# Kernel tuning notes

Hardware: AMD Instinct MI355X
Metric: run time of the kernel (lower is better)

The kernel has to match this reference:

```python
import jax, jax.numpy as jnp
import numpy as np

N_NODES = 8192


def _gcn_norm(edge_index, num_nodes):
    # PyG GCNConv default: add self-loops, symmetric normalization.
    src, dst = edge_index[0], edge_index[1]
    loop = jnp.arange(num_nodes, dtype=src.dtype)
    src = jnp.concatenate([src, loop])
    dst = jnp.concatenate([dst, loop])
    deg = jax.ops.segment_sum(jnp.ones_like(dst, dtype=jnp.float32), dst,
                              num_segments=num_nodes)
    dis = jnp.where(deg > 0, jax.lax.rsqrt(jnp.maximum(deg, 1.0)), 0.0)
    norm = dis[src] * dis[dst]  # [E + N]
    return src, dst, norm


def _gcn_conv(x, W, b, src, dst, norm, num_nodes):
    h = x @ W                           # [N, F_out] dense GEMM
    msg = h[src] * norm[:, None]        # gather + scale, [E+N, F_out]
    out = jax.ops.segment_sum(msg, dst, num_segments=num_nodes)  # scatter-add
    return out + b


def setup_inputs() -> dict:
    key = jax.random.key(0)
    ks = jax.random.split(key, 8)
    N, E, F_in, H1, H2, F_out = N_NODES, 65536, 512, 4096, 1024, 10
    x = jax.random.normal(ks[0], (N, F_in), dtype=jnp.float32)
    edge_index = jax.random.randint(ks[1], (2, E), 0, N, dtype=jnp.int64)
    # Glorot-ish scaled weights
    W1 = jax.random.normal(ks[2], (F_in, H1), dtype=jnp.float32) * (1.0 / np.sqrt(F_in))
    b1 = jnp.zeros((H1,), dtype=jnp.float32)
    W2 = jax.random.normal(ks[3], (H1, H2), dtype=jnp.float32) * (1.0 / np.sqrt(H1))
    b2 = jnp.zeros((H2,), dtype=jnp.float32)
    W3 = jax.random.normal(ks[4], (H2, F_out), dtype=jnp.float32) * (1.0 / np.sqrt(H2))
    b3 = jnp.zeros((F_out,), dtype=jnp.float32)
    return {"x": x, "W1": W1, "b1": b1, "W2": W2, "b2": b2,
            "W3": W3, "b3": b3, "edge_index": edge_index}


def reference(x, W1, b1, W2, b2, W3, b3, edge_index):
    N = N_NODES
    src, dst, norm = _gcn_norm(edge_index, N)
    h = _gcn_conv(x.astype(jnp.float32), W1, b1, src, dst, norm, N)
    h = jax.nn.relu(h)  # dropout is identity in eval mode
    h = _gcn_conv(h, W2, b2, src, dst, norm, N)
    h = jax.nn.relu(h)
    h = _gcn_conv(h, W3, b3, src, dst, norm, N)
    return jax.nn.log_softmax(h, axis=1)
```

## Files before the change

kernel.cpp:

```cpp
#include <hip/hip_runtime.h>
#include <math.h>

#define N_NODES 8192
#define N_EDGES 65536
#define F_IN    512
#define HID1    4096
#define HID2    1024
#define F_OUT   10
#define H3_STRIDE 16
#define W3B_STRIDE 1032

typedef __bf16 bf16x8 __attribute__((ext_vector_type(8)));
typedef float floatx4 __attribute__((ext_vector_type(4)));
typedef float floatx16 __attribute__((ext_vector_type(16)));

static __device__ __forceinline__ unsigned short f2bf(float f) {
    union { float f; unsigned u; } v; v.f = f;
    unsigned r = v.u + 0x7fffu + ((v.u >> 16) & 1u);
    return (unsigned short)(r >> 16);
}
static __device__ __forceinline__ float bf2f(unsigned short u) {
    union { unsigned u; float f; } v; v.u = ((unsigned)u) << 16;
    return v.f;
}
static __device__ __forceinline__ void unpack8(uint4 r, float* f) {
    union { unsigned u; float v; } c;
    c.u = r.x << 16;          f[0] = c.v;
    c.u = r.x & 0xffff0000u;  f[1] = c.v;
    c.u = r.y << 16;          f[2] = c.v;
    c.u = r.y & 0xffff0000u;  f[3] = c.v;
    c.u = r.z << 16;          f[4] = c.v;
    c.u = r.z & 0xffff0000u;  f[5] = c.v;
    c.u = r.w << 16;          f[6] = c.v;
    c.u = r.w & 0xffff0000u;  f[7] = c.v;
}
static __device__ __forceinline__ uint4 pack8(const float* f) {
    uint4 o;
    o.x = (unsigned)f2bf(f[0]) | ((unsigned)f2bf(f[1]) << 16);
    o.y = (unsigned)f2bf(f[2]) | ((unsigned)f2bf(f[3]) << 16);
    o.z = (unsigned)f2bf(f[4]) | ((unsigned)f2bf(f[5]) << 16);
    o.w = (unsigned)f2bf(f[6]) | ((unsigned)f2bf(f[7]) << 16);
    return o;
}

__global__ __launch_bounds__(1024) void hist_scan_kernel(
        const int* __restrict__ ei, int* __restrict__ deg,
        int* __restrict__ row_ptr, int* __restrict__ cnt) {
    __shared__ int hist[N_NODES];
    __shared__ int sums[1024];
    int t = threadIdx.x;
#pragma unroll
    for (int i = 0; i < 8; i++) hist[t + i * 1024] = 0;
    __syncthreads();
#pragma unroll
    for (int i = 0; i < 64; i++) {
        int d = ei[N_EDGES + i * 1024 + t];
        atomicAdd(&hist[d], 1);
    }
    __syncthreads();
    int base = t * 8;
    int local[8], run = 0;
#pragma unroll
    for (int i = 0; i < 8; i++) {
        int dv = hist[base + i];
        deg[base + i] = dv;
        cnt[base + i] = 0;
        local[i] = run; run += dv;
    }
    sums[t] = run;
    __syncthreads();
    for (int off = 1; off < 1024; off <<= 1) {
        int val = (t >= off) ? sums[t - off] : 0;
        __syncthreads();
        sums[t] += val;
        __syncthreads();
    }
    int offset = (t == 0) ? 0 : sums[t - 1];
#pragma unroll
    for (int i = 0; i < 8; i++) row_ptr[base + i] = offset + local[i];
    if (t == 1023) row_ptr[N_NODES] = sums[1023];
}

static __device__ __forceinline__ void transpose_body(
        const float* __restrict__ W, unsigned short* __restrict__ Wt,
        int K, int N, int k0, int n0, int tid, float (*t)[33]) {
    int c = tid & 31, r8 = tid >> 5;
#pragma unroll
    for (int i = 0; i < 4; i++) {
        int r = r8 + i * 8;
        t[r][c] = W[(size_t)(k0 + r) * N + n0 + c];
    }
    __syncthreads();
#pragma unroll
    for (int i = 0; i < 4; i++) {
        int r = r8 + i * 8;
        Wt[(size_t)(n0 + r) * K + k0 + c] = f2bf(t[c][r]);
    }
}

__global__ __launch_bounds__(256) void megaprep_kernel(
        const int* __restrict__ ei, const int* __restrict__ deg,
        const int* __restrict__ row_ptr, int* __restrict__ cnt,
        int* __restrict__ csr_src, float* __restrict__ csr_w,
        const float* __restrict__ x, unsigned short* __restrict__ xb,
        const float* __restrict__ W1, unsigned short* __restrict__ W1t,
        const float* __restrict__ W2, unsigned short* __restrict__ W2t,
        const float* __restrict__ W3, unsigned short* __restrict__ w3b) {
    __shared__ float t[32][33];
    int b = blockIdx.x, tid = threadIdx.x;
    if (b < 256) {
        int e = b * 256 + tid;
        int s = ei[e];
        int d = ei[N_EDGES + e];
        int slot = row_ptr[d] + atomicAdd(&cnt[d], 1);
        csr_src[slot] = s;
        csr_w[slot] = rsqrtf((float)((deg[s] + 1) * (deg[d] + 1)));
    } else if (b < 4352) {
        int i = (b - 256) * 256 + tid;
        float4 a = ((const float4*)x)[i];
        ushort4 o;
        o.x = f2bf(a.x); o.y = f2bf(a.y); o.z = f2bf(a.z); o.w = f2bf(a.w);
        ((ushort4*)xb)[i] = o;
    } else if (b < 6400) {
        int bb = b - 4352;
        transpose_body(W1, W1t, F_IN, HID1, (bb >> 7) * 32, (bb & 127) * 32, tid, t);
    } else if (b < 10496) {
        int bb = b - 6400;
        transpose_body(W2, W2t, HID1, HID2, (bb >> 5) * 32, (bb & 31) * 32, tid, t);
    } else {
        for (int i = tid; i < HID2 * F_OUT; i += 256) {
            int k = i / F_OUT, c = i % F_OUT;
            w3b[c * W3B_STRIDE + k] = f2bf(W3[i]);
        }
    }
}

__global__ __launch_bounds__(256) void agg1_kernel(
        const unsigned short* __restrict__ xb, const int* __restrict__ row_ptr,
        const int* __restrict__ csr_src, const float* __restrict__ csr_w,
        const int* __restrict__ deg, unsigned short* __restrict__ out) {
    int v = blockIdx.x * 4 + (threadIdx.x >> 6);
    int t = threadIdx.x & 63;
    const uint4* xp = (const uint4*)xb;
    float sw = 1.0f / (float)(deg[v] + 1);
    float acc[8], tmp[8];
    unpack8(xp[(size_t)v * 64 + t], tmp);
#pragma unroll
    for (int j = 0; j < 8; j++) acc[j] = sw * tmp[j];
    int e = row_ptr[v], end = row_ptr[v + 1];
    for (; e + 4 <= end; e += 4) {
        int s0 = csr_src[e], s1 = csr_src[e + 1];
        int s2 = csr_src[e + 2], s3 = csr_src[e + 3];
        float w0 = csr_w[e], w1 = csr_w[e + 1];
        float w2 = csr_w[e + 2], w3 = csr_w[e + 3];
        float f0[8], f1[8], f2[8], f3[8];
        unpack8(xp[(size_t)s0 * 64 + t], f0);
        unpack8(xp[(size_t)s1 * 64 + t], f1);
        unpack8(xp[(size_t)s2 * 64 + t], f2);
        unpack8(xp[(size_t)s3 * 64 + t], f3);
#pragma unroll
        for (int j = 0; j < 8; j++)
            acc[j] += w0 * f0[j] + w1 * f1[j] + w2 * f2[j] + w3 * f3[j];
    }
    for (; e < end; e++) {
        int s = csr_src[e];
        float w = csr_w[e];
        float f0[8];
        unpack8(xp[(size_t)s * 64 + t], f0);
#pragma unroll
        for (int j = 0; j < 8; j++) acc[j] += w * f0[j];
    }
    ((uint4*)out)[(size_t)v * 64 + t] = pack8(acc);
}

__global__ __launch_bounds__(256) void agg2_gemm3_kernel(
        const unsigned short* __restrict__ h, const int* __restrict__ row_ptr,
        const int* __restrict__ csr_src, const float* __restrict__ csr_w,
        const int* __restrict__ deg, const float* __restrict__ b2,
        const unsigned short* __restrict__ w3b, float* __restrict__ H3) {
    __shared__ unsigned short w3s[F_OUT * W3B_STRIDE];
    __shared__ float red[4][F_OUT];
    int tid = threadIdx.x;
    for (int i = tid; i < F_OUT * W3B_STRIDE; i += 256) w3s[i] = w3b[i];
    __syncthreads();
    int half = tid >> 7;
    int t = tid & 127;
    int v = blockIdx.x * 2 + half;
    const uint4* hp = (const uint4*)h;
    float sw = 1.0f / (float)(deg[v] + 1);
    float acc[8], tmp[8];
    unpack8(hp[(size_t)v * 128 + t], tmp);
#pragma unroll
    for (int j = 0; j < 8; j++) acc[j] = sw * tmp[j];
    int e = row_ptr[v], end = row_ptr[v + 1];
    for (; e + 4 <= end; e += 4) {
        int s0 = csr_src[e], s1 = csr_src[e + 1];
        int s2 = csr_src[e + 2], s3 = csr_src[e + 3];
        float w0 = csr_w[e], w1 = csr_w[e + 1];
        float w2 = csr_w[e + 2], w3 = csr_w[e + 3];
        float f0[8], f1[8], f2[8], f3[8];
        unpack8(hp[(size_t)s0 * 128 + t], f0);
        unpack8(hp[(size_t)s1 * 128 + t], f1);
        unpack8(hp[(size_t)s2 * 128 + t], f2);
        unpack8(hp[(size_t)s3 * 128 + t], f3);
#pragma unroll
        for (int j = 0; j < 8; j++)
            acc[j] += w0 * f0[j] + w1 * f1[j] + w2 * f2[j] + w3 * f3[j];
    }
    for (; e < end; e++) {
        int s = csr_src[e];
        float w = csr_w[e];
        float f0[8];
        unpack8(hp[(size_t)s * 128 + t], f0);
#pragma unroll
        for (int j = 0; j < 8; j++) acc[j] += w * f0[j];
    }
    float4 b4a = ((const float4*)b2)[t * 2];
    float4 b4b = ((const float4*)b2)[t * 2 + 1];
    acc[0] = fmaxf(acc[0] + b4a.x, 0.0f); acc[1] = fmaxf(acc[1] + b4a.y, 0.0f);
    acc[2] = fmaxf(acc[2] + b4a.z, 0.0f); acc[3] = fmaxf(acc[3] + b4a.w, 0.0f);
    acc[4] = fmaxf(acc[4] + b4b.x, 0.0f); acc[5] = fmaxf(acc[5] + b4b.y, 0.0f);
    acc[6] = fmaxf(acc[6] + b4b.z, 0.0f); acc[7] = fmaxf(acc[7] + b4b.w, 0.0f);

    float partial[F_OUT];
#pragma unroll
    for (int c = 0; c < F_OUT; c++) {
        float wf[8];
        unpack8(*(const uint4*)&w3s[c * W3B_STRIDE + t * 8], wf);
        partial[c] = acc[0] * wf[0] + acc[1] * wf[1] + acc[2] * wf[2] + acc[3] * wf[3]
                   + acc[4] * wf[4] + acc[5] * wf[5] + acc[6] * wf[6] + acc[7] * wf[7];
    }
#pragma unroll
    for (int c = 0; c < F_OUT; c++) {
#pragma unroll
        for (int off = 32; off > 0; off >>= 1)
            partial[c] += __shfl_xor(partial[c], off, 64);
    }
    int wave = tid >> 6, lane = tid & 63;
    if (lane == 0) {
#pragma unroll
        for (int c = 0; c < F_OUT; c++) red[wave][c] = partial[c];
    }
    __syncthreads();
    if (tid < 2 * F_OUT) {
        int hh = tid / F_OUT, c = tid % F_OUT;
        H3[(size_t)(blockIdx.x * 2 + hh) * H3_STRIDE + c] =
            red[hh * 2][c] + red[hh * 2 + 1][c];
    }
}

template <bool OUT_BF16, bool BIAS, bool RELU>
__global__ __launch_bounds__(256) void gemm2_mfma_kernel(
        const unsigned short* __restrict__ A,
        const unsigned short* __restrict__ Bt,
        const float* __restrict__ bias,
        void* __restrict__ C,
        int M, int N, int K) {
    __shared__ unsigned short As[128 * 128];
    __shared__ unsigned short Bs[128 * 128];
    int tid = threadIdx.x;
    int wave = tid >> 6, lane = tid & 63;
    int wm = wave >> 1, wn = wave & 1;
    int GN = N >> 7;
    int b = blockIdx.x;
    int ntile = (b >> 3) % GN;
    int mtile = ((b >> 3) / GN) * 8 + (b & 7);
    int m0 = mtile * 128, n0 = ntile * 128;
    int lrow = lane & 31, lhalf = lane >> 5;

    floatx16 acc[2][2] = {};

    for (int k0 = 0; k0 < K; k0 += 128) {
#pragma unroll
        for (int j = 0; j < 8; j++) {
            int idx = j * 256 + tid;
            int r = idx >> 4;
            int kc = (idx & 15) ^ (r & 15);
            __builtin_amdgcn_global_load_lds(
                (const __attribute__((address_space(1))) void*)(A + (size_t)(m0 + r) * K + k0 + kc * 8),
                (__attribute__((address_space(3))) void*)(&As[idx * 8]), 16, 0, 0);
            __builtin_amdgcn_global_load_lds(
                (const __attribute__((address_space(1))) void*)(Bt + (size_t)(n0 + r) * K + k0 + kc * 8),
                (__attribute__((address_space(3))) void*)(&Bs[idx * 8]), 16, 0, 0);
        }
        __syncthreads();
#pragma unroll
        for (int kk = 0; kk < 8; kk++) {
            bf16x8 af[2], bfr[2];
            int c = kk * 2 + lhalf;
#pragma unroll
            for (int mt = 0; mt < 2; mt++) {
                int R = wm * 64 + mt * 32 + lrow;
                af[mt] = *(const bf16x8*)&As[(R * 16 + (c ^ (R & 15))) * 8];
            }
#pragma unroll
            for (int nt = 0; nt < 2; nt++) {
                int R = wn * 64 + nt * 32 + lrow;
                bfr[nt] = *(const bf16x8*)&Bs[(R * 16 + (c ^ (R & 15))) * 8];
            }
#pragma unroll
            for (int mt = 0; mt < 2; mt++)
#pragma unroll
                for (int nt = 0; nt < 2; nt++)
                    acc[mt][nt] = __builtin_amdgcn_mfma_f32_32x32x16_bf16(
                        af[mt], bfr[nt], acc[mt][nt], 0, 0, 0);
        }
        __syncthreads();
    }

#pragma unroll
    for (int mt = 0; mt < 2; mt++) {
#pragma unroll
        for (int nt = 0; nt < 2; nt++) {
            int col = n0 + wn * 64 + nt * 32 + lrow;
            float bv = BIAS ? bias[col] : 0.0f;
#pragma unroll
            for (int reg = 0; reg < 16; reg++) {
                int row = m0 + wm * 64 + mt * 32 + (reg & 3) + 8 * (reg >> 2) + 4 * lhalf;
                float v = acc[mt][nt][reg] + bv;
                if (RELU) v = fmaxf(v, 0.0f);
                if (OUT_BF16)
                    ((unsigned short*)C)[(size_t)row * N + col] = f2bf(v);
                else
                    ((float*)C)[(size_t)row * N + col] = v;
            }
        }
    }
}

__global__ __launch_bounds__(256, 2) void gemm1_mfma_kernel(
        const unsigned short* __restrict__ A,
        const unsigned short* __restrict__ Bt,
        const float* __restrict__ bias,
        unsigned short* __restrict__ C) {
    __shared__ unsigned short As[256 * 64];
    __shared__ unsigned short Bs[128 * 64];
    const int K = F_IN, N = HID1;
    int tid = threadIdx.x;
    int wave = tid >> 6, lane = tid & 63;
    int wm = wave >> 1, wn = wave & 1;
    int b = blockIdx.x;
    int GN = N >> 7;
    int ntile = (b >> 3) % GN;
    int mtile = ((b >> 3) / GN) * 8 + (b & 7);
    int m0 = mtile * 256, n0 = ntile * 128;
    int lrow = lane & 31, lhalf = lane >> 5;

    floatx16 acc[4][2] = {};

    for (int k0 = 0; k0 < K; k0 += 64) {
#pragma unroll
        for (int j = 0; j < 8; j++) {
            int idx = j * 256 + tid;
            int r = idx >> 3;
            int kc = (idx & 7) ^ (r & 7);
            __builtin_amdgcn_global_load_lds(
                (const __attribute__((address_space(1))) void*)(A + (size_t)(m0 + r) * K + k0 + kc * 8),
                (__attribute__((address_space(3))) void*)(&As[idx * 8]), 16, 0, 0);
        }
#pragma unroll
        for (int j = 0; j < 4; j++) {
            int idx = j * 256 + tid;
            int r = idx >> 3;
            int kc = (idx & 7) ^ (r & 7);
            __builtin_amdgcn_global_load_lds(
                (const __attribute__((address_space(1))) void*)(Bt + (size_t)(n0 + r) * K + k0 + kc * 8),
                (__attribute__((address_space(3))) void*)(&Bs[idx * 8]), 16, 0, 0);
        }
        __syncthreads();
#pragma unroll
        for (int kk = 0; kk < 4; kk++) {
            bf16x8 af[4], bfr[2];
            int c = kk * 2 + lhalf;
#pragma unroll
            for (int mt = 0; mt < 4; mt++) {
                int R = wm * 128 + mt * 32 + lrow;
                af[mt] = *(const bf16x8*)&As[(R * 8 + (c ^ (R & 7))) * 8];
            }
#pragma unroll
            for (int nt = 0; nt < 2; nt++) {
                int R = wn * 64 + nt * 32 + lrow;
                bfr[nt] = *(const bf16x8*)&Bs[(R * 8 + (c ^ (R & 7))) * 8];
            }
#pragma unroll
            for (int mt = 0; mt < 4; mt++)
#pragma unroll
                for (int nt = 0; nt < 2; nt++)
                    acc[mt][nt] = __builtin_amdgcn_mfma_f32_32x32x16_bf16(
                        af[mt], bfr[nt], acc[mt][nt], 0, 0, 0);
        }
        __syncthreads();
    }

#pragma unroll
    for (int mt = 0; mt < 4; mt++) {
#pragma unroll
        for (int nt = 0; nt < 2; nt++) {
            int col = n0 + wn * 64 + nt * 32 + lrow;
            float bv = bias[col];
#pragma unroll
            for (int reg = 0; reg < 16; reg++) {
                int row = m0 + wm * 128 + mt * 32 + (reg & 3) + 8 * (reg >> 2) + 4 * lhalf;
                float v = fmaxf(acc[mt][nt][reg] + bv, 0.0f);
                C[(size_t)row * N + col] = f2bf(v);
            }
        }
    }
}

__global__ void final_kernel(const float* __restrict__ h3, const int* __restrict__ row_ptr,
                             const int* __restrict__ csr_src, const float* __restrict__ csr_w,
                             const int* __restrict__ deg, const float* __restrict__ b3,
                             float* __restrict__ out) {
    int v = blockIdx.x * blockDim.x + threadIdx.x;
    if (v >= N_NODES) return;
    const float4* h4 = (const float4*)h3;
    float sw = 1.0f / (float)(deg[v] + 1);
    float a[12];
    *(float4*)&a[0] = h4[v * 4];
    *(float4*)&a[4] = h4[v * 4 + 1];
    *(float4*)&a[8] = h4[v * 4 + 2];
    float acc[F_OUT];
#pragma unroll
    for (int c = 0; c < F_OUT; c++) acc[c] = b3[c] + sw * a[c];
    int end = row_ptr[v + 1];
    for (int e = row_ptr[v]; e < end; e++) {
        int s = csr_src[e];
        float w = csr_w[e];
        float bsrc[12];
        *(float4*)&bsrc[0] = h4[s * 4];
        *(float4*)&bsrc[4] = h4[s * 4 + 1];
        *(float4*)&bsrc[8] = h4[s * 4 + 2];
#pragma unroll
        for (int c = 0; c < F_OUT; c++) acc[c] += w * bsrc[c];
    }
    float m = acc[0];
#pragma unroll
    for (int c = 1; c < F_OUT; c++) m = fmaxf(m, acc[c]);
    float ssum = 0.0f;
#pragma unroll
    for (int c = 0; c < F_OUT; c++) ssum += expf(acc[c] - m);
    float l = logf(ssum);
#pragma unroll
    for (int c = 0; c < F_OUT; c++) out[v * F_OUT + c] = acc[c] - m - l;
}

extern "C" void kernel_launch(void* const* d_in, const int* in_sizes, int n_in,
                              void* d_out, int out_size, void* d_ws, size_t ws_size,
                              hipStream_t stream) {
    const float* x  = (const float*)d_in[0];
    const float* W1 = (const float*)d_in[1];
    const float* b1 = (const float*)d_in[2];
    const float* W2 = (const float*)d_in[3];
    const float* b2 = (const float*)d_in[4];
    const float* W3 = (const float*)d_in[5];
    const float* b3 = (const float*)d_in[6];
    const int*   ei = (const int*)d_in[7];
    float* out = (float*)d_out;

    char* p = (char*)d_ws;
    int*   deg     = (int*)p;    p += N_NODES * 4;
    int*   cnt     = (int*)p;    p += N_NODES * 4;
    int*   row_ptr = (int*)p;    p += 33024;
    int*   csr_src = (int*)p;    p += N_EDGES * 4;
    float* csr_w   = (float*)p;  p += N_EDGES * 4;
    float* h3      = (float*)p;  p += N_NODES * H3_STRIDE * 4;
    unsigned short* w3b = (unsigned short*)p; p += (F_OUT * W3B_STRIDE * 2 + 255) / 256 * 256;
    unsigned short* xb    = (unsigned short*)p; p += (size_t)N_NODES * F_IN * 2;
    unsigned short* agg_x = (unsigned short*)p; p += (size_t)N_NODES * F_IN * 2;
    unsigned short* W1t   = (unsigned short*)p; p += (size_t)HID1 * F_IN * 2;
    unsigned short* W2t   = (unsigned short*)p; p += (size_t)HID2 * HID1 * 2;
    unsigned short* h1    = (unsigned short*)p; p += (size_t)N_NODES * HID1 * 2;
    unsigned short* h2pre = (unsigned short*)p; p += (size_t)N_NODES * HID2 * 2;

    hist_scan_kernel<<<1, 1024, 0, stream>>>(ei, deg, row_ptr, cnt);
    megaprep_kernel<<<10497, 256, 0, stream>>>(ei, deg, row_ptr, cnt, csr_src, csr_w,
                                               x, xb, W1, W1t, W2, W2t, W3, w3b);

    agg1_kernel<<<N_NODES / 4, 256, 0, stream>>>(xb, row_ptr, csr_src, csr_w, deg, agg_x);
    gemm1_mfma_kernel<<<(HID1 / 128) * (N_NODES / 256), 256, 0, stream>>>(agg_x, W1t, b1, h1);

    gemm2_mfma_kernel<true, false, false><<<(HID2 / 128) * (N_NODES / 128), 256, 0, stream>>>(
        h1, W2t, nullptr, h2pre, N_NODES, HID2, HID1);

    agg2_gemm3_kernel<<<N_NODES / 2, 256, 0, stream>>>(h2pre, row_ptr, csr_src, csr_w,
                                                       deg, b2, w3b, h3);

    final_kernel<<<N_NODES / 256, 256, 0, stream>>>(h3, row_ptr, csr_src, csr_w, deg, b3, out);
}
```

Measured before the change: 287.2 us.

## Replace both GEMMs with a triple-buffered pipelined 128x256 MFMA kernel

Merges the two GEMM kernels into one 512-thread kernel with 128x256 tiles and BK=64. It uses a three-stage LDS ring buffer where global-to-LDS loads for tile t+2 are issued while tile t is computed, tracked with explicit vmcnt waits and raw barriers. It also adds an XCD-aware block swizzle and raises wave priority around the MFMA calls. The aim is to hide global load latency and remove the two full syncs per k-step, at the cost of 144KB of LDS per block (one block per CU) and fragile hand-written waitcnt logic.

After: 297.7 us. +3.7%, slower.

```diff
diff --git a/kernel.cpp b/kernel.cpp
--- a/kernel.cpp
+++ b/kernel.cpp
@@ -249,160 +249,116 @@
     }
 }
 
+#define GP_STAGE(t_, q_) do {                                                  \
+    unsigned short* As_ = lds + (q_) * 24576;                                  \
+    unsigned short* Bs_ = As_ + 8192;                                          \
+    int k0_ = (t_) * 64;                                                       \
+    _Pragma("unroll")                                                          \
+    for (int j = 0; j < 2; j++) {              \
+        int idx = j * 512 + tid;                                               \
+        int r = idx >> 3;                                                      \
+        int kc = (idx & 7) ^ (r & 7);                                          \
+        __builtin_amdgcn_global_load_lds(                                      \
+            (const __attribute__((address_space(1))) void*)(Abase + (size_t)r * K + k0_ + kc * 8), \
+            (__attribute__((address_space(3))) void*)(&As_[idx * 8]), 16, 0, 0); \
+    }                                                                          \
+    _Pragma("unroll")                                                          \
+    for (int j = 0; j < 4; j++) {              \
+        int idx = j * 512 + tid;                                               \
+        int r = idx >> 3;                                                      \
+        int kc = (idx & 7) ^ (r & 7);                                          \
+        __builtin_amdgcn_global_load_lds(                                      \
+            (const __attribute__((address_space(1))) void*)(Bbase + (size_t)r * K + k0_ + kc * 8), \
+            (__attribute__((address_space(3))) void*)(&Bs_[idx * 8]), 16, 0, 0); \
+    }                                                                          \
+} while (0)
+
 template <bool OUT_BF16, bool BIAS, bool RELU>
-__global__ __launch_bounds__(256) void gemm2_mfma_kernel(
+__global__ __launch_bounds__(512) void gemm_pipe_kernel(
         const unsigned short* __restrict__ A,
         const unsigned short* __restrict__ Bt,
         const float* __restrict__ bias,
         void* __restrict__ C,
         int M, int N, int K) {
-    __shared__ unsigned short As[128 * 128];
-    __shared__ unsigned short Bs[128 * 128];
+    __shared__ unsigned short lds[3 * 24576];
     int tid = threadIdx.x;
     int wave = tid >> 6, lane = tid & 63;
-    int wm = wave >> 1, wn = wave & 1;
-    int GN = N >> 7;
+    int wm = wave & 1, wn = wave >> 1;
+    int lrow = lane & 31, lhalf = lane >> 5;
+
+    int nwg = gridDim.x;
+    int cpx = nwg >> 3;
     int b = blockIdx.x;
-    int ntile = (b >> 3) % GN;
-    int mtile = ((b >> 3) / GN) * 8 + (b & 7);
-    int m0 = mtile * 128, n0 = ntile * 128;
-    int lrow = lane & 31, lhalf = lane >> 5;
+    int swz = (b & 7) * cpx + (b >> 3);
+    int nm = M >> 7;
+    int ntile = swz / nm;
+    int mtile = swz - ntile * nm;
+
+    const unsigned short* Abase = A + (size_t)mtile * 128 * K;
+    const unsigned short* Bbase = Bt + (size_t)ntile * 256 * K;
 
     floatx16 acc[2][2] = {};
-
-    for (int k0 = 0; k0 < K; k0 += 128) {
-#pragma unroll
-        for (int j = 0; j < 8; j++) {
-            int idx = j * 256 + tid;
-            int r = idx >> 4;
-            int kc = (idx & 15) ^ (r & 15);
-            __builtin_amdgcn_global_load_lds(
-                (const __attribute__((address_space(1))) void*)(A + (size_t)(m0 + r) * K + k0 + kc * 8),
-                (__attribute__((address_space(3))) void*)(&As[idx * 8]), 16, 0, 0);
-            __builtin_amdgcn_global_load_lds(
-                (const __attribute__((address_space(1))) void*)(Bt + (size_t)(n0 + r) * K + k0 + kc * 8),
-                (__attribute__((address_space(3))) void*)(&Bs[idx * 8]), 16, 0, 0);
-        }
-        __syncthreads();
-#pragma unroll
-        for (int kk = 0; kk < 8; kk++) {
+    int NT = K >> 6;
+
+    GP_STAGE(0, 0);
+    GP_STAGE(1, 1);
+    asm volatile("s_waitcnt vmcnt(6)" ::: "memory");
+    __builtin_amdgcn_s_barrier();
+
+    int q = 0, qn = 2;
+    for (int t = 0; t < NT; t++) {
+        unsigned short* As_ = lds + q * 24576;
+        unsigned short* Bs_ = As_ + 8192;
+#pragma unroll
+        for (int kk = 0; kk < 4; kk++) {
             bf16x8 af[2], bfr[2];
             int c = kk * 2 + lhalf;
 #pragma unroll
             for (int mt = 0; mt < 2; mt++) {
                 int R = wm * 64 + mt * 32 + lrow;
-                af[mt] = *(const bf16x8*)&As[(R * 16 + (c ^ (R & 15))) * 8];
+                af[mt] = *(const bf16x8*)&As_[(R * 8 + (c ^ (R & 7))) * 8];
             }
 #pragma unroll
             for (int nt = 0; nt < 2; nt++) {
                 int R = wn * 64 + nt * 32 + lrow;
-                bfr[nt] = *(const bf16x8*)&Bs[(R * 16 + (c ^ (R & 15))) * 8];
+                bfr[nt] = *(const bf16x8*)&Bs_[(R * 8 + (c ^ (R & 7))) * 8];
             }
+            if (kk == 0 && t + 2 < NT) {
+                GP_STAGE(t + 2, qn);
+            }
+            __builtin_amdgcn_s_setprio(1);
 #pragma unroll
             for (int mt = 0; mt < 2; mt++)
 #pragma unroll
                 for (int nt = 0; nt < 2; nt++)
                     acc[mt][nt] = __builtin_amdgcn_mfma_f32_32x32x16_bf16(
                         af[mt], bfr[nt], acc[mt][nt], 0, 0, 0);
+            __builtin_amdgcn_s_setprio(0);
         }
-        __syncthreads();
+        if (t + 2 < NT)
+            asm volatile("s_waitcnt vmcnt(6)" ::: "memory");
+        else
+            asm volatile("s_waitcnt vmcnt(0)" ::: "memory");
+        __builtin_amdgcn_s_barrier();
+        q = (q == 2) ? 0 : q + 1;
+        qn = (qn == 2) ? 0 : qn + 1;
     }
 
 #pragma unroll
     for (int mt = 0; mt < 2; mt++) {
 #pragma unroll
         for (int nt = 0; nt < 2; nt++) {
-            int col = n0 + wn * 64 + nt * 32 + lrow;
+            int col = ntile * 256 + wn * 64 + nt * 32 + lrow;
             float bv = BIAS ? bias[col] : 0.0f;
 #pragma unroll
             for (int reg = 0; reg < 16; reg++) {
-                int row = m0 + wm * 64 + mt * 32 + (reg & 3) + 8 * (reg >> 2) + 4 * lhalf;
+                int row = mtile * 128 + wm * 64 + mt * 32 + (reg & 3) + 8 * (reg >> 2) + 4 * lhalf;
                 float v = acc[mt][nt][reg] + bv;
                 if (RELU) v = fmaxf(v, 0.0f);
                 if (OUT_BF16)
                     ((unsigned short*)C)[(size_t)row * N + col] = f2bf(v);
                 else
                     ((float*)C)[(size_t)row * N + col] = v;
-            }
-        }
-    }
-}
-
-__global__ __launch_bounds__(256, 2) void gemm1_mfma_kernel(
-        const unsigned short* __restrict__ A,
-        const unsigned short* __restrict__ Bt,
-        const float* __restrict__ bias,
-        unsigned short* __restrict__ C) {
-    __shared__ unsigned short As[256 * 64];
-    __shared__ unsigned short Bs[128 * 64];
-    const int K = F_IN, N = HID1;
-    int tid = threadIdx.x;
-    int wave = tid >> 6, lane = tid & 63;
-    int wm = wave >> 1, wn = wave & 1;
-    int b = blockIdx.x;
-    int GN = N >> 7;
-    int ntile = (b >> 3) % GN;
-    int mtile = ((b >> 3) / GN) * 8 + (b & 7);
-    int m0 = mtile * 256, n0 = ntile * 128;
-    int lrow = lane & 31, lhalf = lane >> 5;
-
-    floatx16 acc[4][2] = {};
-
-    for (int k0 = 0; k0 < K; k0 += 64) {
-#pragma unroll
-        for (int j = 0; j < 8; j++) {
-            int idx = j * 256 + tid;
-            int r = idx >> 3;
-            int kc = (idx & 7) ^ (r & 7);
-            __builtin_amdgcn_global_load_lds(
-                (const __attribute__((address_space(1))) void*)(A + (size_t)(m0 + r) * K + k0 + kc * 8),
-                (__attribute__((address_space(3))) void*)(&As[idx * 8]), 16, 0, 0);
-        }
-#pragma unroll
-        for (int j = 0; j < 4; j++) {
-            int idx = j * 256 + tid;
-            int r = idx >> 3;
-            int kc = (idx & 7) ^ (r & 7);
-            __builtin_amdgcn_global_load_lds(
-                (const __attribute__((address_space(1))) void*)(Bt + (size_t)(n0 + r) * K + k0 + kc * 8),
-                (__attribute__((address_space(3))) void*)(&Bs[idx * 8]), 16, 0, 0);
-        }
-        __syncthreads();
-#pragma unroll
-        for (int kk = 0; kk < 4; kk++) {
-            bf16x8 af[4], bfr[2];
-            int c = kk * 2 + lhalf;
-#pragma unroll
-            for (int mt = 0; mt < 4; mt++) {
-                int R = wm * 128 + mt * 32 + lrow;
-                af[mt] = *(const bf16x8*)&As[(R * 8 + (c ^ (R & 7))) * 8];
-            }
-#pragma unroll
-            for (int nt = 0; nt < 2; nt++) {
-                int R = wn * 64 + nt * 32 + lrow;
-                bfr[nt] = *(const bf16x8*)&Bs[(R * 8 + (c ^ (R & 7))) * 8];
-            }
-#pragma unroll
-            for (int mt = 0; mt < 4; mt++)
-#pragma unroll
-                for (int nt = 0; nt < 2; nt++)
-                    acc[mt][nt] = __builtin_amdgcn_mfma_f32_32x32x16_bf16(
-                        af[mt], bfr[nt], acc[mt][nt], 0, 0, 0);
-        }
-        __syncthreads();
-    }
-
-#pragma unroll
-    for (int mt = 0; mt < 4; mt++) {
-#pragma unroll
-        for (int nt = 0; nt < 2; nt++) {
-            int col = n0 + wn * 64 + nt * 32 + lrow;
-            float bv = bias[col];
-#pragma unroll
-            for (int reg = 0; reg < 16; reg++) {
-                int row = m0 + wm * 128 + mt * 32 + (reg & 3) + 8 * (reg >> 2) + 4 * lhalf;
-                float v = fmaxf(acc[mt][nt][reg] + bv, 0.0f);
-                C[(size_t)row * N + col] = f2bf(v);
             }
         }
     }
@@ -478,9 +434,10 @@
                                                x, xb, W1, W1t, W2, W2t, W3, w3b);
 
     agg1_kernel<<<N_NODES / 4, 256, 0, stream>>>(xb, row_ptr, csr_src, csr_w, deg, agg_x);
-    gemm1_mfma_kernel<<<(HID1 / 128) * (N_NODES / 256), 256, 0, stream>>>(agg_x, W1t, b1, h1);
-
-    gemm2_mfma_kernel<true, false, false><<<(HID2 / 128) * (N_NODES / 128), 256, 0, stream>>>(
+    gemm_pipe_kernel<true, true, true><<<(N_NODES / 128) * (HID1 / 256), 512, 0, stream>>>(
+        agg_x, W1t, b1, h1, N_NODES, HID1, F_IN);
+
+    gemm_pipe_kernel<true, false, false><<<(N_NODES / 128) * (HID2 / 256), 512, 0, stream>>>(
         h1, W2t, nullptr, h2pre, N_NODES, HID2, HID1);
 
     agg2_gemm3_kernel<<<N_NODES / 2, 256, 0, stream>>>(h2pre, row_ptr, csr_src, csr_w,
```

## Pipeline gemm2 with triple-buffered LDS and larger 256x128 tiles

Applied to the files above, without the earlier changes.

Replaces the single-buffered gemm2 kernel with a triple-buffered version that issues global-to-LDS loads two K-steps ahead and interleaves them with the MFMA work. Each wave now computes 128x64 instead of 64x64, so each B fragment is reused across more A rows, and s_setprio raises priority around the MFMA blocks. Per-block synchronisation now relies on explicit vmcnt waits instead of two __syncthreads per step. The 144KB LDS footprint limits occupancy to one block per CU, and the doubled accumulators raise register pressure.

Measured after the change: 284.1 us. About the same (-1.1%).

```diff
diff --git a/kernel.cpp b/kernel.cpp
--- a/kernel.cpp
+++ b/kernel.cpp
@@ -249,74 +249,114 @@
     }
 }
 
+#define G2_STAGE_A(t_, q_, j0_) do {                                           \
+    unsigned short* As_ = lds + (q_) * 24576;                                  \
+    int k0_ = (t_) * 64;                                                       \
+    _Pragma("unroll")                                                          \
+    for (int j = (j0_); j < (j0_) + 4; j++) {      \
+        int idx = j * 256 + tid;                                               \
+        int r = idx >> 3;                                                      \
+        int kc = (idx & 7) ^ (r & 7);                                          \
+        __builtin_amdgcn_global_load_lds(                                      \
+            (const __attribute__((address_space(1))) void*)(Abase + (size_t)r * K + k0_ + kc * 8), \
+            (__attribute__((address_space(3))) void*)(&As_[idx * 8]), 16, 0, 0); \
+    }                                                                          \
+} while (0)
+
+#define G2_STAGE_B(t_, q_) do {                                                \
+    unsigned short* Bs_ = lds + (q_) * 24576 + 16384;                          \
+    int k0_ = (t_) * 64;                                                       \
+    _Pragma("unroll")                                                          \
+    for (int j = 0; j < 4; j++) {                  \
+        int idx = j * 256 + tid;                                               \
+        int r = idx >> 3;                                                      \
+        int kc = (idx & 7) ^ (r & 7);                                          \
+        __builtin_amdgcn_global_load_lds(                                      \
+            (const __attribute__((address_space(1))) void*)(Bbase + (size_t)r * K + k0_ + kc * 8), \
+            (__attribute__((address_space(3))) void*)(&Bs_[idx * 8]), 16, 0, 0); \
+    }                                                                          \
+} while (0)
+
 template <bool OUT_BF16, bool BIAS, bool RELU>
-__global__ __launch_bounds__(256) void gemm2_mfma_kernel(
+__global__ __launch_bounds__(256, 1) void gemm2_pipe_kernel(
         const unsigned short* __restrict__ A,
         const unsigned short* __restrict__ Bt,
         const float* __restrict__ bias,
         void* __restrict__ C,
         int M, int N, int K) {
-    __shared__ unsigned short As[128 * 128];
-    __shared__ unsigned short Bs[128 * 128];
+    __shared__ unsigned short lds[3 * 24576];
     int tid = threadIdx.x;
     int wave = tid >> 6, lane = tid & 63;
     int wm = wave >> 1, wn = wave & 1;
+    int lrow = lane & 31, lhalf = lane >> 5;
+
     int GN = N >> 7;
     int b = blockIdx.x;
     int ntile = (b >> 3) % GN;
     int mtile = ((b >> 3) / GN) * 8 + (b & 7);
-    int m0 = mtile * 128, n0 = ntile * 128;
-    int lrow = lane & 31, lhalf = lane >> 5;
-
-    floatx16 acc[2][2] = {};
-
-    for (int k0 = 0; k0 < K; k0 += 128) {
-#pragma unroll
-        for (int j = 0; j < 8; j++) {
-            int idx = j * 256 + tid;
-            int r = idx >> 4;
-            int kc = (idx & 15) ^ (r & 15);
-            __builtin_amdgcn_global_load_lds(
-                (const __attribute__((address_space(1))) void*)(A + (size_t)(m0 + r) * K + k0 + kc * 8),
-                (__attribute__((address_space(3))) void*)(&As[idx * 8]), 16, 0, 0);
-            __builtin_amdgcn_global_load_lds(
-                (const __attribute__((address_space(1))) void*)(Bt + (size_t)(n0 + r) * K + k0 + kc * 8),
-                (__attribute__((address_space(3))) void*)(&Bs[idx * 8]), 16, 0, 0);
-        }
-        __syncthreads();
-#pragma unroll
-        for (int kk = 0; kk < 8; kk++) {
-            bf16x8 af[2], bfr[2];
+    int m0 = mtile * 256, n0 = ntile * 128;
+
+    const unsigned short* Abase = A + (size_t)m0 * K;
+    const unsigned short* Bbase = Bt + (size_t)n0 * K;
+
+    floatx16 acc[4][2] = {};
+    int NT = K >> 6;
+
+    G2_STAGE_A(0, 0, 0); G2_STAGE_A(0, 0, 4); G2_STAGE_B(0, 0);
+    G2_STAGE_A(1, 1, 0); G2_STAGE_A(1, 1, 4); G2_STAGE_B(1, 1);
+    asm volatile("s_waitcnt vmcnt(12)" ::: "memory");
+    __builtin_amdgcn_s_barrier();
+
+    int q = 0, qn = 2;
+    for (int t = 0; t < NT; t++) {
+        unsigned short* As_ = lds + q * 24576;
+        unsigned short* Bs_ = As_ + 16384;
+#pragma unroll
+        for (int kk = 0; kk < 4; kk++) {
+            bf16x8 af[4], bfr[2];
             int c = kk * 2 + lhalf;
 #pragma unroll
-            for (int mt = 0; mt < 2; mt++) {
-                int R = wm * 64 + mt * 32 + lrow;
-                af[mt] = *(const bf16x8*)&As[(R * 16 + (c ^ (R & 15))) * 8];
+            for (int mt = 0; mt < 4; mt++) {
+                int R = wm * 128 + mt * 32 + lrow;
+                af[mt] = *(const bf16x8*)&As_[(R * 8 + (c ^ (R & 7))) * 8];
             }
 #pragma unroll
             for (int nt = 0; nt < 2; nt++) {
                 int R = wn * 64 + nt * 32 + lrow;
-                bfr[nt] = *(const bf16x8*)&Bs[(R * 16 + (c ^ (R & 15))) * 8];
-            }
-#pragma unroll
-            for (int mt = 0; mt < 2; mt++)
+                bfr[nt] = *(const bf16x8*)&Bs_[(R * 8 + (c ^ (R & 7))) * 8];
+            }
+            if (t + 2 < NT) {
+                if (kk == 0)      G2_STAGE_A(t + 2, qn, 0);
+                else if (kk == 1) G2_STAGE_A(t + 2, qn, 4);
+                else if (kk == 2) G2_STAGE_B(t + 2, qn);
+            }
+            __builtin_amdgcn_s_setprio(1);
+#pragma unroll
+            for (int mt = 0; mt < 4; mt++)
 #pragma unroll
                 for (int nt = 0; nt < 2; nt++)
                     acc[mt][nt] = __builtin_amdgcn_mfma_f32_32x32x16_bf16(
                         af[mt], bfr[nt], acc[mt][nt], 0, 0, 0);
-        }
-        __syncthreads();
-    }
-
-#pragma unroll
-    for (int mt = 0; mt < 2; mt++) {
+            __builtin_amdgcn_s_setprio(0);
+        }
+        if (t + 2 < NT)
+            asm volatile("s_waitcnt vmcnt(12)" ::: "memory");
+        else
+            asm volatile("s_waitcnt vmcnt(0)" ::: "memory");
+        __builtin_amdgcn_s_barrier();
+        q = (q == 2) ? 0 : q + 1;
+        qn = (qn == 2) ? 0 : qn + 1;
+    }
+
+#pragma unroll
+    for (int mt = 0; mt < 4; mt++) {
 #pragma unroll
         for (int nt = 0; nt < 2; nt++) {
             int col = n0 + wn * 64 + nt * 32 + lrow;
             float bv = BIAS ? bias[col] : 0.0f;
 #pragma unroll
             for (int reg = 0; reg < 16; reg++) {
-                int row = m0 + wm * 64 + mt * 32 + (reg & 3) + 8 * (reg >> 2) + 4 * lhalf;
+                int row = m0 + wm * 128 + mt * 32 + (reg & 3) + 8 * (reg >> 2) + 4 * lhalf;
                 float v = acc[mt][nt][reg] + bv;
                 if (RELU) v = fmaxf(v, 0.0f);
                 if (OUT_BF16)
@@ -480,7 +520,7 @@
     agg1_kernel<<<N_NODES / 4, 256, 0, stream>>>(xb, row_ptr, csr_src, csr_w, deg, agg_x);
     gemm1_mfma_kernel<<<(HID1 / 128) * (N_NODES / 256), 256, 0, stream>>>(agg_x, W1t, b1, h1);
 
-    gemm2_mfma_kernel<true, false, false><<<(HID2 / 128) * (N_NODES / 128), 256, 0, stream>>>(
+    gemm2_pipe_kernel<true, false, false><<<(N_NODES / 256) * (HID2 / 128), 256, 0, stream>>>(
         h1, W2t, nullptr, h2pre, N_NODES, HID2, HID1);
 
     agg2_gemm3_kernel<<<N_NODES / 2, 256, 0, stream>>>(h2pre, row_ptr, csr_src, csr_w,
```

## Replace gemm1 with double-buffered 256x256 pipelined MFMA kernel; vectorize histogram loads

Applied to the files above, without the earlier changes.

Replaces the first GEMM with a 512-thread kernel using 256x256 tiles, double-buffered LDS and global-to-LDS prefetch of the next K slice interleaved with MFMA work. It uses explicit vmcnt waits, s_barrier and setprio, so loads overlap compute instead of a full sync per K step. The degree histogram now reads destination indices as int4 to cut load instructions. The new kernel uses 128KB of LDS per block and fragile manual wait counts, which may limit occupancy or risk races.

New measurement: 284.0 us. Within noise of the previous version (-1.1%).

```diff
diff --git a/kernel.cpp b/kernel.cpp
--- a/kernel.cpp
+++ b/kernel.cpp
@@ -52,10 +52,14 @@
 #pragma unroll
     for (int i = 0; i < 8; i++) hist[t + i * 1024] = 0;
     __syncthreads();
-#pragma unroll
-    for (int i = 0; i < 64; i++) {
-        int d = ei[N_EDGES + i * 1024 + t];
-        atomicAdd(&hist[d], 1);
+    const int4* ei4 = (const int4*)(ei + N_EDGES);
+#pragma unroll
+    for (int i = 0; i < 16; i++) {
+        int4 d4 = ei4[i * 1024 + t];
+        atomicAdd(&hist[d4.x], 1);
+        atomicAdd(&hist[d4.y], 1);
+        atomicAdd(&hist[d4.z], 1);
+        atomicAdd(&hist[d4.w], 1);
     }
     __syncthreads();
     int base = t * 8;
@@ -249,6 +253,118 @@
     }
 }
 
+#define P8_STAGE(mat_, kh_, dd_, base_, k0_) do {                              \
+    unsigned short* L_ = lds + ((dd_) * 4 + (mat_) * 2 + (kh_)) * 8192;        \
+    _Pragma("unroll")                                                          \
+    for (int j = 0; j < 2; j++) {                                              \
+        int slot = j * 512 + tid;                                              \
+        int s4 = slot >> 4, cs = slot & 15;                                    \
+        int csp = cs ^ (s4 & 3);                                               \
+        int grow = s4 * 4 + (csp >> 2);                                        \
+        int gcol = (csp & 3) * 8;                                              \
+        __builtin_amdgcn_global_load_lds(                                      \
+            (const __attribute__((address_space(1))) void*)((base_) + (size_t)grow * K + (k0_) + (kh_) * 32 + gcol), \
+            (__attribute__((address_space(3))) void*)(&L_[slot * 8]), 16, 0, 0); \
+    }                                                                          \
+} while (0)
+
+#define P8_OFF(R_, lc_) ((((R_) >> 2) * 128) + (((((R_) & 3) << 2) | (lc_)) ^ (((R_) >> 2) & 3)) * 8)
+
+__global__ __launch_bounds__(512, 2) void gemm1_pipe8_kernel(
+        const unsigned short* __restrict__ A,
+        const unsigned short* __restrict__ Bt,
+        const float* __restrict__ bias,
+        unsigned short* __restrict__ C) {
+    __shared__ unsigned short lds[65536];
+    const int K = F_IN, N = HID1;
+    int tid = threadIdx.x;
+    int wave = tid >> 6, lane = tid & 63;
+    int wm = wave >> 2, wn = wave & 3;
+    int lrow = lane & 31, lhalf = lane >> 5;
+
+    int b = blockIdx.x;
+    int GN = HID1 >> 8;
+    int ntile = (b >> 3) % GN;
+    int mtile = ((b >> 3) / GN) * 8 + (b & 7);
+    int m0 = mtile * 256, n0 = ntile * 256;
+
+    const unsigned short* Abase = A + (size_t)m0 * K;
+    const unsigned short* Bbase = Bt + (size_t)n0 * K;
+
+    floatx16 acc[4][2] = {};
+    const int NT = K >> 6;
+
+    P8_STAGE(0, 0, 0, Abase, 0);
+    P8_STAGE(1, 0, 0, Bbase, 0);
+    P8_STAGE(0, 1, 0, Abase, 0);
+    P8_STAGE(1, 1, 0, Bbase, 0);
+    asm volatile("s_waitcnt vmcnt(4)" ::: "memory");
+    __builtin_amdgcn_s_barrier();
+
+    for (int t = 0; t < NT; t++) {
+        int d = t & 1, dn = d ^ 1;
+        int k1 = (t + 1) * 64;
+#pragma unroll
+        for (int kk = 0; kk < 4; kk++) {
+            if (kk == 2) {
+                if (t + 1 < NT)
+                    asm volatile("s_waitcnt vmcnt(4)" ::: "memory");
+                else
+                    asm volatile("s_waitcnt vmcnt(0)" ::: "memory");
+                __builtin_amdgcn_s_barrier();
+            }
+            int kh = kk >> 1;
+            int lc0 = (kk & 1) * 2 + lhalf;
+            const unsigned short* Ak = lds + (d * 4 + kh) * 8192;
+            const unsigned short* Bk = lds + (d * 4 + 2 + kh) * 8192;
+            bf16x8 af[4], bfr[2];
+#pragma unroll
+            for (int mt = 0; mt < 4; mt++) {
+                int R = wm * 128 + mt * 32 + lrow;
+                af[mt] = *(const bf16x8*)&Ak[P8_OFF(R, lc0)];
+            }
+#pragma unroll
+            for (int nt = 0; nt < 2; nt++) {
+                int R = wn * 64 + nt * 32 + lrow;
+                bfr[nt] = *(const bf16x8*)&Bk[P8_OFF(R, lc0)];
+            }
+            if (t + 1 < NT) {
+                if (kk == 0)      P8_STAGE(0, 0, dn, Abase, k1);
+                else if (kk == 1) P8_STAGE(1, 0, dn, Bbase, k1);
+                else if (kk == 2) P8_STAGE(0, 1, dn, Abase, k1);
+                else              P8_STAGE(1, 1, dn, Bbase, k1);
+            }
+            __builtin_amdgcn_s_barrier();
+            __builtin_amdgcn_s_setprio(1);
+#pragma unroll
+            for (int mt = 0; mt < 4; mt++)
+#pragma unroll
+                for (int nt = 0; nt < 2; nt++)
+                    acc[mt][nt] = __builtin_amdgcn_mfma_f32_32x32x16_bf16(
+                        af[mt], bfr[nt], acc[mt][nt], 0, 0, 0);
+            __builtin_amdgcn_s_setprio(0);
+            if (kk == 0 || kk == 2) __builtin_amdgcn_s_barrier();
+        }
+        asm volatile("s_waitcnt vmcnt(4)" ::: "memory");
+        __builtin_amdgcn_s_barrier();
+    }
+
+#pragma unroll
+    for (int mt = 0; mt < 4; mt++) {
+#pragma unroll
+        for (int nt = 0; nt < 2; nt++) {
+            int col = n0 + wn * 64 + nt * 32 + lrow;
+            float bv = bias[col];
+#pragma unroll
+            for (int reg = 0; reg < 16; reg++) {
+                int row = m0 + wm * 128 + mt * 32 + (reg & 3) + 8 * (reg >> 2) + 4 * lhalf;
+                float v = fmaxf(acc[mt][nt][reg] + bv, 0.0f);
+                C[(size_t)row * N + col] = f2bf(v);
+            }
+        }
+    }
+}
+
 template <bool OUT_BF16, bool BIAS, bool RELU>
 __global__ __launch_bounds__(256) void gemm2_mfma_kernel(
         const unsigned short* __restrict__ A,
@@ -328,86 +444,6 @@
     }
 }
 
-__global__ __launch_bounds__(256, 2) void gemm1_mfma_kernel(
-        const unsigned short* __restrict__ A,
-        const unsigned short* __restrict__ Bt,
-        const float* __restrict__ bias,
-        unsigned short* __restrict__ C) {
-    __shared__ unsigned short As[256 * 64];
-    __shared__ unsigned short Bs[128 * 64];
-    const int K = F_IN, N = HID1;
-    int tid = threadIdx.x;
-    int wave = tid >> 6, lane = tid & 63;
-    int wm = wave >> 1, wn = wave & 1;
-    int b = blockIdx.x;
-    int GN = N >> 7;
-    int ntile = (b >> 3) % GN;
-    int mtile = ((b >> 3) / GN) * 8 + (b & 7);
-    int m0 = mtile * 256, n0 = ntile * 128;
-    int lrow = lane & 31, lhalf = lane >> 5;
-
-    floatx16 acc[4][2] = {};
-
-    for (int k0 = 0; k0 < K; k0 += 64) {
-#pragma unroll
-        for (int j = 0; j < 8; j++) {
-            int idx = j * 256 + tid;
-            int r = idx >> 3;
-            int kc = (idx & 7) ^ (r & 7);
-            __builtin_amdgcn_global_load_lds(
-                (const __attribute__((address_space(1))) void*)(A + (size_t)(m0 + r) * K + k0 + kc * 8),
-                (__attribute__((address_space(3))) void*)(&As[idx * 8]), 16, 0, 0);
-        }
-#pragma unroll
-        for (int j = 0; j < 4; j++) {
-            int idx = j * 256 + tid;
-            int r = idx >> 3;
-            int kc = (idx & 7) ^ (r & 7);
-            __builtin_amdgcn_global_load_lds(
-                (const __attribute__((address_space(1))) void*)(Bt + (size_t)(n0 + r) * K + k0 + kc * 8),
-                (__attribute__((address_space(3))) void*)(&Bs[idx * 8]), 16, 0, 0);
-        }
-        __syncthreads();
-#pragma unroll
-        for (int kk = 0; kk < 4; kk++) {
-            bf16x8 af[4], bfr[2];
-            int c = kk * 2 + lhalf;
-#pragma unroll
-            for (int mt = 0; mt < 4; mt++) {
-                int R = wm * 128 + mt * 32 + lrow;
-                af[mt] = *(const bf16x8*)&As[(R * 8 + (c ^ (R & 7))) * 8];
-            }
-#pragma unroll
-            for (int nt = 0; nt < 2; nt++) {
-                int R = wn * 64 + nt * 32 + lrow;
-                bfr[nt] = *(const bf16x8*)&Bs[(R * 8 + (c ^ (R & 7))) * 8];
-            }
-#pragma unroll
-            for (int mt = 0; mt < 4; mt++)
-#pragma unroll
-                for (int nt = 0; nt < 2; nt++)
-                    acc[mt][nt] = __builtin_amdgcn_mfma_f32_32x32x16_bf16(
-                        af[mt], bfr[nt], acc[mt][nt], 0, 0, 0);
-        }
-        __syncthreads();
-    }
-
-#pragma unroll
-    for (int mt = 0; mt < 4; mt++) {
-#pragma unroll
-        for (int nt = 0; nt < 2; nt++) {
-            int col = n0 + wn * 64 + nt * 32 + lrow;
-            float bv = bias[col];
-#pragma unroll
-            for (int reg = 0; reg < 16; reg++) {
-                int row = m0 + wm * 128 + mt * 32 + (reg & 3) + 8 * (reg >> 2) + 4 * lhalf;
-                float v = fmaxf(acc[mt][nt][reg] + bv, 0.0f);
-                C[(size_t)row * N + col] = f2bf(v);
-            }
-        }
-    }
-}
-
 __global__ void final_kernel(const float* __restrict__ h3, const int* __restrict__ row_ptr,
                              const int* __restrict__ csr_src, const float* __restrict__ csr_w,
                              const int* __restrict__ deg, const float* __restrict__ b3,
@@ -478,7 +514,8 @@
                                                x, xb, W1, W1t, W2, W2t, W3, w3b);
 
     agg1_kernel<<<N_NODES / 4, 256, 0, stream>>>(xb, row_ptr, csr_src, csr_w, deg, agg_x);
-    gemm1_mfma_kernel<<<(HID1 / 128) * (N_NODES / 256), 256, 0, stream>>>(agg_x, W1t, b1, h1);
+    gemm1_pipe8_kernel<<<(N_NODES / 256) * (HID1 / 256) * 8 / 8, 512, 0, stream>>>(
+        agg_x, W1t, b1, h1);
 
     gemm2_mfma_kernel<true, false, false><<<(HID2 / 128) * (N_NODES / 128), 256, 0, stream>>>(
         h1, W2t, nullptr, h2pre, N_NODES, HID2, HID1);
```
